# Performance work log

Hardware: AMD Instinct MI355X
Metric: run time of the kernel (lower is better)

The kernel has to match this reference:

```python
import jax, jax.numpy as jnp
import numpy as np

N, M, FDIM, EDIM, H, HEADS = 8192, 8192, 128, 128, 64, 4
NEG = -1e9


def setup_inputs() -> dict:
    key = jax.random.key(0)
    ks = jax.random.split(key, 6)
    F0 = jax.random.normal(ks[0], (N, FDIM), dtype=jnp.float32)
    E0 = jax.random.normal(ks[1], (M, EDIM), dtype=jnp.float32)
    A = jax.random.randint(ks[2], (N, M), 0, 2, dtype=jnp.int32)
    Wf = jax.random.normal(ks[3], (HEADS, FDIM, H), dtype=jnp.float32) * 0.05
    We = jax.random.normal(ks[4], (HEADS, EDIM, H), dtype=jnp.float32) * 0.05
    a = jax.random.normal(ks[5], (HEADS, H), dtype=jnp.float32) * 0.05
    return {"F0": F0, "E0": E0, "A": A, "Wf": Wf, "We": We, "a": a}


def reference(F0, E0, A, Wf, We, a):
    # Per-head linear projections: h=head, n/m=nodes, d=hidden
    F1 = jnp.einsum('nf,hfd->hnd', F0, Wf)   # [H, N, D]
    E1 = jnp.einsum('me,hed->hmd', E0, We)   # [H, M, D]
    # Additive GAT scores: (h_src @ a) + (h_dst @ a), broadcast over the grid
    e_src = jnp.einsum('hnd,hd->hn', F1, a)  # [H, N]
    e_dst = jnp.einsum('hmd,hd->hm', E1, a)  # [H, M]
    e = jax.nn.leaky_relu(e_src[:, :, None] + e_dst[:, None, :], negative_slope=0.2)
    e = jnp.where(A[None, :, :] > 0, e, NEG)
    alpha = jax.nn.softmax(e, axis=-1)       # [H, N, M]
    h_prime = jnp.einsum('hnm,hmd->hnd', alpha, E1)  # [H, N, D]
    out = jnp.mean(h_prime, axis=0)          # mean over heads -> [N, D]
    return jax.nn.softmax(out, axis=-1)
```

## Files before the change

kernel.cpp:

```cpp
#include <hip/hip_runtime.h>
#include <hip/hip_fp16.h>

#define NN 8192
#define MM 8192
#define FD 128
#define EDm 128
#define HD 64
#define NH 4
#define NTILE 32

typedef float f32x4 __attribute__((ext_vector_type(4)));
typedef _Float16 h16x8 __attribute__((ext_vector_type(8)));
typedef unsigned int u32;

__global__ void k_esrc(const float* __restrict__ F0, const float* __restrict__ Wf,
                       const float* __restrict__ a, float* __restrict__ esrc) {
  __shared__ float vfL[NH * FD];
  int t = threadIdx.x;
#pragma unroll
  for (int r = 0; r < 2; ++r) {
    int idx = t + r * 256;
    int h = idx >> 7, f = idx & 127;
    const float* w = Wf + (size_t)(h * FD + f) * HD;
    const float* av = a + h * HD;
    float s = 0.f;
#pragma unroll
    for (int d = 0; d < HD; ++d) s += w[d] * av[d];
    vfL[idx] = s;
  }
  __syncthreads();
  int g = blockIdx.x * 256 + t;
  int n = g >> 2, h = g & 3;
  const float4* fr = (const float4*)(F0 + (size_t)n * FD);
  const float4* vr = (const float4*)(vfL + h * FD);
  float s = 0.f;
#pragma unroll
  for (int i = 0; i < FD / 4; ++i) {
    float4 x = fr[i], y = vr[i];
    s += x.x * y.x + x.y * y.y + x.z * y.z + x.w * y.w;
  }
  esrc[h * NN + n] = s;
}

__global__ void k_e1(const float* __restrict__ E0, const float* __restrict__ We,
                     const float* __restrict__ a, uint4* __restrict__ Bp,
                     _Float16* __restrict__ edh, _Float16* __restrict__ ed2h) {
  int wid = (blockIdx.x * blockDim.x + threadIdx.x) >> 6;
  int lane = threadIdx.x & 63;
  int h = wid >> 10;
  int mg = wid & 1023;
  int m = mg * 8;
  const float* we = We + (size_t)h * EDm * HD + lane;
  const float* e0r = E0 + (size_t)m * EDm;
  float ac[8] = {};
#pragma unroll 4
  for (int e = 0; e < EDm; ++e) {
    float wv = we[e * HD];
#pragma unroll
    for (int j = 0; j < 8; ++j) ac[j] += e0r[j * EDm + e] * wv;
  }
  int mc = mg >> 2, quad = mg & 3, dt = lane >> 4, col = lane & 15;
  union { h16x8 v; uint4 u; } hv;
#pragma unroll
  for (int j = 0; j < 8; ++j) hv.v[j] = (_Float16)ac[j];
  Bp[(((size_t)h * 256 + mc) * 4 + dt) * 64 + quad * 16 + col] = hv.u;

  float av = a[h * HD + lane];
  float d[8];
#pragma unroll
  for (int j = 0; j < 8; ++j) d[j] = ac[j] * av;
#pragma unroll
  for (int o = 32; o; o >>= 1)
#pragma unroll
    for (int j = 0; j < 8; ++j) d[j] += __shfl_xor(d[j], o);
  if (lane == 0) {
    const float L2E = 1.4426950408889634f;
    union { h16x8 v; uint4 u; } e1, e2;
#pragma unroll
    for (int j = 0; j < 8; ++j) {
      e1.v[j] = (_Float16)exp2f(d[j] * L2E);
      e2.v[j] = (_Float16)exp2f(0.2f * d[j] * L2E);
    }
    *(uint4*)(edh + (size_t)h * MM + m) = e1.u;
    *(uint4*)(ed2h + (size_t)h * MM + m) = e2.u;
  }
}

__device__ __forceinline__ u32 hm2b(u32 w, int bit) {
  return (((w >> bit) & 1u) | (((w >> (bit + 1)) & 1u) << 16)) * 0xffffu;
}

__global__ __launch_bounds__(1024, 4) void k_main(
    const int* __restrict__ A, const uint4* __restrict__ Bp,
    const float* __restrict__ esrc, const _Float16* __restrict__ edh,
    const _Float16* __restrict__ ed2h, float* __restrict__ out) {
  __shared__ __align__(16) char smem[41472];
  u32* bits = (u32*)smem;
  float* Hsum = (float*)smem;
  float* Dsum = (float*)(smem + 32768);
  float* hp = (float*)(smem + 33280);

  const int t = threadIdx.x;
  const int lane = t & 63;
  const int wv = t >> 6;
  const int h = wv & 3;
  const int q = wv >> 2;
  const int col = lane & 15;
  const int quad = lane >> 4;
  const int qs = quad * 8;
  const int n0 = blockIdx.x * NTILE;
  const float L2E = 1.4426950408889634f;

  {
    const int r0 = wv * 2, r1 = r0 + 1;
    const int* a0p = A + (size_t)(n0 + r0) * MM + lane;
    const int* a1p = A + (size_t)(n0 + r1) * MM + lane;
    for (int c8 = 0; c8 < 16; ++c8) {
      int v0[8], v1[8];
#pragma unroll
      for (int k = 0; k < 8; ++k)
        v0[k] = __builtin_nontemporal_load(a0p + (c8 * 8 + k) * 64);
#pragma unroll
      for (int k = 0; k < 8; ++k)
        v1[k] = __builtin_nontemporal_load(a1p + (c8 * 8 + k) * 64);
#pragma unroll
      for (int k = 0; k < 8; ++k) {
        int c = c8 * 8 + k;
        unsigned long long b = __ballot(v0[k] > 0);
        if (lane == 0) bits[r0 * 257 + 2 * c] = (u32)b;
        if (lane == 32) bits[r0 * 257 + 2 * c + 1] = (u32)(b >> 32);
      }
#pragma unroll
      for (int k = 0; k < 8; ++k) {
        int c = c8 * 8 + k;
        unsigned long long b = __ballot(v1[k] > 0);
        if (lane == 0) bits[r1 * 257 + 2 * c] = (u32)b;
        if (lane == 32) bits[r1 * 257 + 2 * c + 1] = (u32)(b >> 32);
      }
    }
  }
  __syncthreads();

  float s0 = esrc[h * NN + n0 + col];
  float s1 = esrc[h * NN + n0 + 16 + col];
  _Float16 e80 = (_Float16)exp2f(0.8f * s0 * L2E);
  _Float16 e81 = (_Float16)exp2f(0.8f * s1 * L2E);
  h16x8 es80 = {e80, e80, e80, e80, e80, e80, e80, e80};
  h16x8 es81 = {e81, e81, e81, e81, e81, e81, e81, e81};

  f32x4 acc[2][4] = {};
  f32x4 accd[2] = {};
  const h16x8 ones = {(_Float16)1.f, (_Float16)1.f, (_Float16)1.f, (_Float16)1.f,
                      (_Float16)1.f, (_Float16)1.f, (_Float16)1.f, (_Float16)1.f};

  const u32* w0p = bits + col * 257 + q * 64;
  const u32* w1p = bits + (col + 16) * 257 + q * 64;
  const _Float16* edp = edh + (size_t)h * MM + q * 2048 + qs;
  const _Float16* e2p = ed2h + (size_t)h * MM + q * 2048 + qs;
  const uint4* bp = Bp + ((size_t)h * 256 + q * 64) * 256 + lane;

  u32 aw0 = w0p[0], aw1 = w1p[0];
  h16x8 edv = *(const h16x8*)edp;
  h16x8 e2v = *(const h16x8*)e2p;
  uint4 bu0 = bp[0], bu1 = bp[64], bu2 = bp[128], bu3 = bp[192];

  for (int it = 0; it < 64; ++it) {
    u32 naw0 = 0, naw1 = 0;
    h16x8 nedv = {}, ne2v = {};
    uint4 nb0 = {}, nb1 = {}, nb2 = {}, nb3 = {};
    if (it < 63) {
      naw0 = w0p[it + 1];
      naw1 = w1p[it + 1];
      nedv = *(const h16x8*)(edp + (it + 1) * 32);
      ne2v = *(const h16x8*)(e2p + (it + 1) * 32);
      nb0 = bp[(it + 1) * 256];
      nb1 = bp[(it + 1) * 256 + 64];
      nb2 = bp[(it + 1) * 256 + 128];
      nb3 = bp[(it + 1) * 256 + 192];
    }

    uint4 m0, m1;
    m0.x = hm2b(aw0, qs);     m0.y = hm2b(aw0, qs + 2);
    m0.z = hm2b(aw0, qs + 4); m0.w = hm2b(aw0, qs + 6);
    m1.x = hm2b(aw1, qs);     m1.y = hm2b(aw1, qs + 2);
    m1.z = hm2b(aw1, qs + 4); m1.w = hm2b(aw1, qs + 6);

    union { h16x8 v; uint4 u; } w0, w1, b0, b1, b2, b3;
    b0.u = bu0; b1.u = bu1; b2.u = bu2; b3.u = bu3;
    w0.v = __builtin_elementwise_max(edv * es80, e2v);
    w1.v = __builtin_elementwise_max(edv * es81, e2v);
    w0.u.x &= m0.x; w0.u.y &= m0.y; w0.u.z &= m0.z; w0.u.w &= m0.w;
    w1.u.x &= m1.x; w1.u.y &= m1.y; w1.u.z &= m1.z; w1.u.w &= m1.w;

    acc[0][0] = __builtin_amdgcn_mfma_f32_16x16x32_f16(w0.v, b0.v, acc[0][0], 0, 0, 0);
    acc[1][0] = __builtin_amdgcn_mfma_f32_16x16x32_f16(w1.v, b0.v, acc[1][0], 0, 0, 0);
    acc[0][1] = __builtin_amdgcn_mfma_f32_16x16x32_f16(w0.v, b1.v, acc[0][1], 0, 0, 0);
    acc[1][1] = __builtin_amdgcn_mfma_f32_16x16x32_f16(w1.v, b1.v, acc[1][1], 0, 0, 0);
    acc[0][2] = __builtin_amdgcn_mfma_f32_16x16x32_f16(w0.v, b2.v, acc[0][2], 0, 0, 0);
    acc[1][2] = __builtin_amdgcn_mfma_f32_16x16x32_f16(w1.v, b2.v, acc[1][2], 0, 0, 0);
    acc[0][3] = __builtin_amdgcn_mfma_f32_16x16x32_f16(w0.v, b3.v, acc[0][3], 0, 0, 0);
    acc[1][3] = __builtin_amdgcn_mfma_f32_16x16x32_f16(w1.v, b3.v, acc[1][3], 0, 0, 0);
    accd[0] = __builtin_amdgcn_mfma_f32_16x16x32_f16(w0.v, ones, accd[0], 0, 0, 0);
    accd[1] = __builtin_amdgcn_mfma_f32_16x16x32_f16(w1.v, ones, accd[1], 0, 0, 0);

    aw0 = naw0; aw1 = naw1; edv = nedv; e2v = ne2v;
    bu0 = nb0; bu1 = nb1; bu2 = nb2; bu3 = nb3;
  }
  __syncthreads();

  for (int i = t; i < 8320; i += 1024) Hsum[i] = 0.f;
  __syncthreads();

  float* Hh = Hsum + h * 2048;
#pragma unroll
  for (int rt = 0; rt < 2; ++rt) {
#pragma unroll
    for (int dt = 0; dt < 4; ++dt)
#pragma unroll
      for (int r2 = 0; r2 < 4; ++r2)
        atomicAdd(&Hh[(rt * 16 + quad * 4 + r2) * 64 + dt * 16 + col],
                  acc[rt][dt][r2]);
    if (col == 0) {
#pragma unroll
      for (int r2 = 0; r2 < 4; ++r2)
        atomicAdd(&Dsum[h * 32 + rt * 16 + quad * 4 + r2], accd[rt][r2]);
    }
  }
  __syncthreads();

  for (int i = t; i < 2048; i += 1024) {
    int r = i >> 6;
    float v = 0.f;
#pragma unroll
    for (int hh = 0; hh < 4; ++hh) v += Hsum[hh * 2048 + i] / Dsum[hh * 32 + r];
    hp[i] = 0.25f * v;
  }
  __syncthreads();

#pragma unroll
  for (int i = 0; i < 2; ++i) {
    int r = wv * 2 + i;
    float v = hp[r * 64 + lane];
    float mx = v;
#pragma unroll
    for (int o = 32; o; o >>= 1) mx = fmaxf(mx, __shfl_xor(mx, o));
    float p = exp2f((v - mx) * L2E);
    float sm = p;
#pragma unroll
    for (int o = 32; o; o >>= 1) sm += __shfl_xor(sm, o);
    out[(size_t)(n0 + r) * HD + lane] = p / sm;
  }
}

extern "C" void kernel_launch(void* const* d_in, const int* in_sizes, int n_in,
                              void* d_out, int out_size, void* d_ws, size_t ws_size,
                              hipStream_t stream) {
  const float* F0 = (const float*)d_in[0];
  const float* E0 = (const float*)d_in[1];
  const int* A = (const int*)d_in[2];
  const float* Wf = (const float*)d_in[3];
  const float* We = (const float*)d_in[4];
  const float* a = (const float*)d_in[5];
  float* out = (float*)d_out;

  char* w = (char*)d_ws;
  float* esrc = (float*)w;        w += (size_t)NH * NN * 4;
  _Float16* edh = (_Float16*)w;   w += (size_t)NH * MM * 2;
  _Float16* ed2h = (_Float16*)w;  w += (size_t)NH * MM * 2;
  uint4* Bp = (uint4*)w;          w += (size_t)NH * HD * MM * 2;

  k_esrc<<<(NH * NN) / 256 / 4, 256, 0, stream>>>(F0, Wf, a, esrc);
  k_e1<<<(NH * MM / 8) / 4, 256, 0, stream>>>(E0, We, a, Bp, edh, ed2h);
  k_main<<<NN / NTILE, 1024, 0, stream>>>(A, Bp, esrc, edh, ed2h, out);
}
```

Measured before the change: 485.8 us.

## Replicate B operand into 8 copies selected per block, peel final loop iteration

k_e1 now writes the packed fp16 E1 matrix (4 MiB) eight times with nontemporal stores, and each k_main block reads the copy chosen by blockIdx&7. The likely aim is to spread the heavily shared B reads across more memory channels or XCD-local caches, since consecutive blocks are probably assigned to different XCDs on MI355X. The main loop also peels its last iteration to drop the conditional prefetch, and the mask AND becomes one vector op. The cost is 28 MiB of extra writes in k_e1 and a larger workspace.

```diff
diff --git a/kernel.cpp b/kernel.cpp
--- a/kernel.cpp
+++ b/kernel.cpp
@@ -8,10 +8,12 @@
 #define HD 64
 #define NH 4
 #define NTILE 32
+#define BPCOPY 262144
 
 typedef float f32x4 __attribute__((ext_vector_type(4)));
 typedef _Float16 h16x8 __attribute__((ext_vector_type(8)));
 typedef unsigned int u32;
+typedef u32 u32x4 __attribute__((ext_vector_type(4)));
 
 __global__ void k_esrc(const float* __restrict__ F0, const float* __restrict__ Wf,
                        const float* __restrict__ a, float* __restrict__ esrc) {
@@ -43,7 +45,7 @@
 }
 
 __global__ void k_e1(const float* __restrict__ E0, const float* __restrict__ We,
-                     const float* __restrict__ a, uint4* __restrict__ Bp,
+                     const float* __restrict__ a, u32x4* __restrict__ Bp,
                      _Float16* __restrict__ edh, _Float16* __restrict__ ed2h) {
   int wid = (blockIdx.x * blockDim.x + threadIdx.x) >> 6;
   int lane = threadIdx.x & 63;
@@ -60,10 +62,13 @@
     for (int j = 0; j < 8; ++j) ac[j] += e0r[j * EDm + e] * wv;
   }
   int mc = mg >> 2, quad = mg & 3, dt = lane >> 4, col = lane & 15;
-  union { h16x8 v; uint4 u; } hv;
+  union { h16x8 v; u32x4 u; } hv;
 #pragma unroll
   for (int j = 0; j < 8; ++j) hv.v[j] = (_Float16)ac[j];
-  Bp[(((size_t)h * 256 + mc) * 4 + dt) * 64 + quad * 16 + col] = hv.u;
+  size_t boff = (((size_t)h * 256 + mc) * 4 + dt) * 64 + quad * 16 + col;
+#pragma unroll
+  for (int c = 0; c < 8; ++c)
+    __builtin_nontemporal_store(hv.u, Bp + (size_t)c * BPCOPY + boff);
 
   float av = a[h * HD + lane];
   float d[8];
@@ -75,14 +80,14 @@
     for (int j = 0; j < 8; ++j) d[j] += __shfl_xor(d[j], o);
   if (lane == 0) {
     const float L2E = 1.4426950408889634f;
-    union { h16x8 v; uint4 u; } e1, e2;
+    union { h16x8 v; u32x4 u; } e1, e2;
 #pragma unroll
     for (int j = 0; j < 8; ++j) {
       e1.v[j] = (_Float16)exp2f(d[j] * L2E);
       e2.v[j] = (_Float16)exp2f(0.2f * d[j] * L2E);
     }
-    *(uint4*)(edh + (size_t)h * MM + m) = e1.u;
-    *(uint4*)(ed2h + (size_t)h * MM + m) = e2.u;
+    *(u32x4*)(edh + (size_t)h * MM + m) = e1.u;
+    *(u32x4*)(ed2h + (size_t)h * MM + m) = e2.u;
   }
 }
 
@@ -91,7 +96,7 @@
 }
 
 __global__ __launch_bounds__(1024, 4) void k_main(
-    const int* __restrict__ A, const uint4* __restrict__ Bp,
+    const int* __restrict__ A, const u32x4* __restrict__ Bp,
     const float* __restrict__ esrc, const _Float16* __restrict__ edh,
     const _Float16* __restrict__ ed2h, float* __restrict__ out) {
   __shared__ __align__(16) char smem[41472];
@@ -157,55 +162,63 @@
   const u32* w1p = bits + (col + 16) * 257 + q * 64;
   const _Float16* edp = edh + (size_t)h * MM + q * 2048 + qs;
   const _Float16* e2p = ed2h + (size_t)h * MM + q * 2048 + qs;
-  const uint4* bp = Bp + ((size_t)h * 256 + q * 64) * 256 + lane;
+  const u32x4* bp = Bp + (size_t)(blockIdx.x & 7) * BPCOPY +
+                    ((size_t)h * 256 + q * 64) * 256 + lane;
 
   u32 aw0 = w0p[0], aw1 = w1p[0];
   h16x8 edv = *(const h16x8*)edp;
   h16x8 e2v = *(const h16x8*)e2p;
-  uint4 bu0 = bp[0], bu1 = bp[64], bu2 = bp[128], bu3 = bp[192];
-
-  for (int it = 0; it < 64; ++it) {
-    u32 naw0 = 0, naw1 = 0;
-    h16x8 nedv = {}, ne2v = {};
-    uint4 nb0 = {}, nb1 = {}, nb2 = {}, nb3 = {};
-    if (it < 63) {
-      naw0 = w0p[it + 1];
-      naw1 = w1p[it + 1];
-      nedv = *(const h16x8*)(edp + (it + 1) * 32);
-      ne2v = *(const h16x8*)(e2p + (it + 1) * 32);
-      nb0 = bp[(it + 1) * 256];
-      nb1 = bp[(it + 1) * 256 + 64];
-      nb2 = bp[(it + 1) * 256 + 128];
-      nb3 = bp[(it + 1) * 256 + 192];
-    }
-
-    uint4 m0, m1;
-    m0.x = hm2b(aw0, qs);     m0.y = hm2b(aw0, qs + 2);
-    m0.z = hm2b(aw0, qs + 4); m0.w = hm2b(aw0, qs + 6);
-    m1.x = hm2b(aw1, qs);     m1.y = hm2b(aw1, qs + 2);
-    m1.z = hm2b(aw1, qs + 4); m1.w = hm2b(aw1, qs + 6);
-
-    union { h16x8 v; uint4 u; } w0, w1, b0, b1, b2, b3;
-    b0.u = bu0; b1.u = bu1; b2.u = bu2; b3.u = bu3;
-    w0.v = __builtin_elementwise_max(edv * es80, e2v);
-    w1.v = __builtin_elementwise_max(edv * es81, e2v);
-    w0.u.x &= m0.x; w0.u.y &= m0.y; w0.u.z &= m0.z; w0.u.w &= m0.w;
-    w1.u.x &= m1.x; w1.u.y &= m1.y; w1.u.z &= m1.z; w1.u.w &= m1.w;
-
-    acc[0][0] = __builtin_amdgcn_mfma_f32_16x16x32_f16(w0.v, b0.v, acc[0][0], 0, 0, 0);
-    acc[1][0] = __builtin_amdgcn_mfma_f32_16x16x32_f16(w1.v, b0.v, acc[1][0], 0, 0, 0);
-    acc[0][1] = __builtin_amdgcn_mfma_f32_16x16x32_f16(w0.v, b1.v, acc[0][1], 0, 0, 0);
-    acc[1][1] = __builtin_amdgcn_mfma_f32_16x16x32_f16(w1.v, b1.v, acc[1][1], 0, 0, 0);
-    acc[0][2] = __builtin_amdgcn_mfma_f32_16x16x32_f16(w0.v, b2.v, acc[0][2], 0, 0, 0);
-    acc[1][2] = __builtin_amdgcn_mfma_f32_16x16x32_f16(w1.v, b2.v, acc[1][2], 0, 0, 0);
-    acc[0][3] = __builtin_amdgcn_mfma_f32_16x16x32_f16(w0.v, b3.v, acc[0][3], 0, 0, 0);
-    acc[1][3] = __builtin_amdgcn_mfma_f32_16x16x32_f16(w1.v, b3.v, acc[1][3], 0, 0, 0);
-    accd[0] = __builtin_amdgcn_mfma_f32_16x16x32_f16(w0.v, ones, accd[0], 0, 0, 0);
-    accd[1] = __builtin_amdgcn_mfma_f32_16x16x32_f16(w1.v, ones, accd[1], 0, 0, 0);
-
-    aw0 = naw0; aw1 = naw1; edv = nedv; e2v = ne2v;
-    bu0 = nb0; bu1 = nb1; bu2 = nb2; bu3 = nb3;
-  }
+  u32x4 bu0 = bp[0], bu1 = bp[64], bu2 = bp[128], bu3 = bp[192];
+
+#define STEP(PREFETCH)                                                         \
+  {                                                                            \
+    u32 naw0, naw1;                                                            \
+    h16x8 nedv, ne2v;                                                          \
+    u32x4 nb0, nb1, nb2, nb3;                                                  \
+    if (PREFETCH) {                                                            \
+      naw0 = w0p[it + 1];                                                      \
+      naw1 = w1p[it + 1];                                                      \
+      nedv = *(const h16x8*)(edp + (it + 1) * 32);                             \
+      ne2v = *(const h16x8*)(e2p + (it + 1) * 32);                             \
+      nb0 = bp[(it + 1) * 256];                                                \
+      nb1 = bp[(it + 1) * 256 + 64];                                           \
+      nb2 = bp[(it + 1) * 256 + 128];                                          \
+      nb3 = bp[(it + 1) * 256 + 192];                                          \
+    }                                                                          \
+    u32x4 m0, m1;                                                              \
+    m0.x = hm2b(aw0, qs);     m0.y = hm2b(aw0, qs + 2);                        \
+    m0.z = hm2b(aw0, qs + 4); m0.w = hm2b(aw0, qs + 6);                        \
+    m1.x = hm2b(aw1, qs);     m1.y = hm2b(aw1, qs + 2);                        \
+    m1.z = hm2b(aw1, qs + 4); m1.w = hm2b(aw1, qs + 6);                        \
+    union { h16x8 v; u32x4 u; } w0, w1, b0, b1, b2, b3;                        \
+    b0.u = bu0; b1.u = bu1; b2.u = bu2; b3.u = bu3;                            \
+    w0.v = __builtin_elementwise_max(edv * es80, e2v);                         \
+    w1.v = __builtin_elementwise_max(edv * es81, e2v);                         \
+    w0.u &= m0;                                                                \
+    w1.u &= m1;                                                                \
+    acc[0][0] = __builtin_amdgcn_mfma_f32_16x16x32_f16(w0.v, b0.v, acc[0][0], 0, 0, 0); \
+    acc[1][0] = __builtin_amdgcn_mfma_f32_16x16x32_f16(w1.v, b0.v, acc[1][0], 0, 0, 0); \
+    acc[0][1] = __builtin_amdgcn_mfma_f32_16x16x32_f16(w0.v, b1.v, acc[0][1], 0, 0, 0); \
+    acc[1][1] = __builtin_amdgcn_mfma_f32_16x16x32_f16(w1.v, b1.v, acc[1][1], 0, 0, 0); \
+    acc[0][2] = __builtin_amdgcn_mfma_f32_16x16x32_f16(w0.v, b2.v, acc[0][2], 0, 0, 0); \
+    acc[1][2] = __builtin_amdgcn_mfma_f32_16x16x32_f16(w1.v, b2.v, acc[1][2], 0, 0, 0); \
+    acc[0][3] = __builtin_amdgcn_mfma_f32_16x16x32_f16(w0.v, b3.v, acc[0][3], 0, 0, 0); \
+    acc[1][3] = __builtin_amdgcn_mfma_f32_16x16x32_f16(w1.v, b3.v, acc[1][3], 0, 0, 0); \
+    accd[0] = __builtin_amdgcn_mfma_f32_16x16x32_f16(w0.v, ones, accd[0], 0, 0, 0);     \
+    accd[1] = __builtin_amdgcn_mfma_f32_16x16x32_f16(w1.v, ones, accd[1], 0, 0, 0);     \
+    if (PREFETCH) {                                                            \
+      aw0 = naw0; aw1 = naw1; edv = nedv; e2v = ne2v;                          \
+      bu0 = nb0; bu1 = nb1; bu2 = nb2; bu3 = nb3;                              \
+    }                                                                          \
+  }
+
+  for (int it = 0; it < 63; ++it) STEP(1)
+  {
+    const int it = 63;
+    (void)it;
+    STEP(0)
+  }
+#undef STEP
   __syncthreads();
 
   for (int i = t; i < 8320; i += 1024) Hsum[i] = 0.f;
@@ -267,7 +280,7 @@
   float* esrc = (float*)w;        w += (size_t)NH * NN * 4;
   _Float16* edh = (_Float16*)w;   w += (size_t)NH * MM * 2;
   _Float16* ed2h = (_Float16*)w;  w += (size_t)NH * MM * 2;
-  uint4* Bp = (uint4*)w;          w += (size_t)NH * HD * MM * 2;
+  u32x4* Bp = (u32x4*)w;          w += (size_t)8 * BPCOPY * 16;
 
   k_esrc<<<(NH * NN) / 256 / 4, 256, 0, stream>>>(F0, Wf, a, esrc);
   k_e1<<<(NH * MM / 8) / 4, 256, 0, stream>>>(E0, We, a, Bp, edh, ed2h);
```

Result: slower. 502.9 us (+3.5%).
